# Kernel tuning notes

Hardware: AMD Instinct MI355X
Metric: run time of the kernel (lower is better)

Reference implementation:

```python
import jax, jax.numpy as jnp
import numpy as np


def _generate_anchors(anc, grid):
    # anc: (A,2) = (w,h); grid: (B,H,W,2) = (x,y) centers
    # -> anchors (B,A,H,W,4) = (x_tl, y_tl, x_br, y_br)
    centers = jnp.concatenate([grid, grid], axis=-1)[:, None, :, :, :]  # (B,1,H,W,4)
    half = 0.5 * jnp.stack([-anc[:, 0], -anc[:, 1], anc[:, 0], anc[:, 1]], axis=-1)  # (A,4)
    return centers + half[None, :, None, None, :]


def _generate_proposals_yolo(anchors, offsets):
    # anchors, offsets: (B,A,H,W,4) -> proposals (B,A,H,W,4)
    x_ca = 0.5 * (anchors[..., 0] + anchors[..., 2])
    y_ca = 0.5 * (anchors[..., 1] + anchors[..., 3])
    wa = anchors[..., 2] - anchors[..., 0]
    ha = anchors[..., 3] - anchors[..., 1]
    # YOLO transform: center shift is additive, size is log-space scale
    x_cp = x_ca + offsets[..., 0]
    y_cp = y_ca + offsets[..., 1]
    wp = wa * jnp.exp(offsets[..., 2])
    hp = ha * jnp.exp(offsets[..., 3])
    return jnp.stack([x_cp - 0.5 * wp, y_cp - 0.5 * hp,
                      x_cp + 0.5 * wp, y_cp + 0.5 * hp], axis=-1)


def _iou(proposals, bboxes):
    # proposals: (B,A,H,W,4); bboxes: (B,N,5) -> iou_mat (B, A*H*W, N)
    B = proposals.shape[0]
    p = proposals.reshape(B, -1, 1, 4)          # (B, AHW, 1, 4)
    b = bboxes[:, None, :, :4]                   # (B, 1,  N, 4)
    tl = jnp.maximum(p[..., :2], b[..., :2])     # (B, AHW, N, 2)
    br = jnp.minimum(p[..., 2:], b[..., 2:])
    no_inter = (tl[..., 0] > br[..., 0]) | (tl[..., 1] > br[..., 1])
    aoi = (br[..., 0] - tl[..., 0]) * (br[..., 1] - tl[..., 1])
    aoi = jnp.where(no_inter, 0.0, aoi)
    aop = (p[..., 2] - p[..., 0]) * (p[..., 3] - p[..., 1])  # (B, AHW, 1)
    aob = (b[..., 2] - b[..., 0]) * (b[..., 3] - b[..., 1])  # (B, 1,  N)
    return aoi / (aop + aob - aoi)


def setup_inputs() -> dict:
    key = jax.random.key(0)
    k1, k2, k3, k4 = jax.random.split(key, 4)
    B, A, H, W, N = 16, 9, 56, 56, 64
    anc = jax.random.uniform(k1, (A, 2), dtype=jnp.float32)          # anchor (w,h) shapes
    grid = jax.random.uniform(k2, (B, H, W, 2), dtype=jnp.float32)   # cell centers
    offsets = jax.random.normal(k3, (B, A, H, W, 4), dtype=jnp.float32)
    bboxes = jax.random.uniform(k4, (B, N, 5), dtype=jnp.float32)    # GT boxes (x1,y1,x2,y2,cls)
    return {"anc": anc, "grid": grid, "offsets": offsets, "bboxes": bboxes}


def reference(anc, grid, offsets, bboxes):
    anchors = _generate_anchors(anc, grid)
    proposals = _generate_proposals_yolo(anchors, offsets)
    iou_mat = _iou(proposals, bboxes)
    return iou_mat
```

## Files before the change

### kernel.cpp

```cpp
#include <hip/hip_runtime.h>
#include <hip/hip_bf16.h>


constexpr int B_ = 16;
constexpr int A_ = 9;
constexpr int H_ = 56;
constexpr int W_ = 56;
constexpr int N_ = 64;
constexpr int HW_ = H_ * W_;
constexpr int P_ = A_ * HW_;
constexpr int BLOCK = 192;
constexpr int BLKS_PER_BATCH = P_ / BLOCK;

__global__ __launch_bounds__(BLOCK) void ssd_iou_kernel(
    const float* __restrict__ anc,
    const float* __restrict__ grid,
    const float* __restrict__ offsets,
    const float* __restrict__ bboxes,
    float* __restrict__ out)
{
    __shared__ float4 s_box[BLOCK];
    __shared__ float  s_aop[BLOCK];

    const int t  = threadIdx.x;
    const int b  = blockIdx.x / BLKS_PER_BATCH;
    const int lb = blockIdx.x - b * BLKS_PER_BATCH;
    const int p0 = lb * BLOCK;

    {
        const int lp = p0 + t;
        const int a  = lp / HW_;
        const int hw = lp - a * HW_;
        const int gp = b * P_ + lp;

        const float4 off = reinterpret_cast<const float4*>(offsets)[gp];
        const float2 g   = reinterpret_cast<const float2*>(grid)[b * HW_ + hw];
        const float  aw  = anc[2 * a + 0];
        const float  ah  = anc[2 * a + 1];

        const float xc = g.x + off.x;
        const float yc = g.y + off.y;
        const float wp = aw * __expf(off.z);
        const float hp = ah * __expf(off.w);

        float4 box;
        box.x = xc - 0.5f * wp;
        box.y = yc - 0.5f * hp;
        box.z = xc + 0.5f * wp;
        box.w = yc + 0.5f * hp;
        s_box[t] = box;
        s_aop[t] = wp * hp;
    }
    __syncthreads();

    const int wave = t >> 6;
    const int lane = t & 63;

    const float* bb = bboxes + ((size_t)(b * N_ + lane)) * 5;
    const float bx0 = bb[0];
    const float by0 = bb[1];
    const float bx1 = bb[2];
    const float by1 = bb[3];
    const float aob = (bx1 - bx0) * (by1 - by0);

    const int   pbase = wave * 64;
    float* orow = out + ((size_t)(b * P_ + p0 + pbase)) * N_ + lane;

    #pragma unroll 8
    for (int j = 0; j < 64; ++j) {
        const float4 pr  = s_box[pbase + j];
        const float  aop = s_aop[pbase + j];

        const float tlx = fmaxf(pr.x, bx0);
        const float tly = fmaxf(pr.y, by0);
        const float brx = fminf(pr.z, bx1);
        const float bry = fminf(pr.w, by1);

        const float iw  = fmaxf(brx - tlx, 0.0f);
        const float ih  = fmaxf(bry - tly, 0.0f);
        const float aoi = iw * ih;

        const float denom = aop + aob - aoi;
        const float iou   = aoi * __frcp_rn(denom);

        __builtin_nontemporal_store(iou, orow + (size_t)j * N_);
    }
}

extern "C" void kernel_launch(void* const* d_in, const int* in_sizes, int n_in,
                              void* d_out, int out_size, void* d_ws, size_t ws_size,
                              hipStream_t stream) {
    const float* anc     = (const float*)d_in[0];
    const float* grid    = (const float*)d_in[1];
    const float* offsets = (const float*)d_in[2];
    const float* bboxes  = (const float*)d_in[3];
    float* out = (float*)d_out;

    const int nblocks = B_ * BLKS_PER_BATCH;
    ssd_iou_kernel<<<nblocks, BLOCK, 0, stream>>>(anc, grid, offsets, bboxes, out);
}
```

Before: 136.9 us.

## Vectorize IoU output stores to 128-bit by giving each lane four boxes

Each lane now computes four consecutive GT boxes for one proposal and writes them with a single 128-bit nontemporal store, in place of one 32-bit store per lane per proposal. The per-proposal area is recomputed from the shared box, so the separate shared-memory area array is gone. The correctly rounded reciprocal is replaced with the raw hardware rcp builtin. This aims to cut store instruction count on a write-bound kernel, at the cost of more registers per lane and slightly different rounding in the division.

```diff
diff --git a/kernel.cpp b/kernel.cpp
--- a/kernel.cpp
+++ b/kernel.cpp
@@ -12,6 +12,8 @@
 constexpr int BLOCK = 192;
 constexpr int BLKS_PER_BATCH = P_ / BLOCK;
 
+typedef float floatx4 __attribute__((ext_vector_type(4)));
+
 __global__ __launch_bounds__(BLOCK) void ssd_iou_kernel(
     const float* __restrict__ anc,
     const float* __restrict__ grid,
@@ -20,7 +22,6 @@
     float* __restrict__ out)
 {
     __shared__ float4 s_box[BLOCK];
-    __shared__ float  s_aop[BLOCK];
 
     const int t  = threadIdx.x;
     const int b  = blockIdx.x / BLKS_PER_BATCH;
@@ -49,41 +50,51 @@
         box.z = xc + 0.5f * wp;
         box.w = yc + 0.5f * hp;
         s_box[t] = box;
-        s_aop[t] = wp * hp;
     }
     __syncthreads();
 
     const int wave = t >> 6;
     const int lane = t & 63;
+    const int q    = lane >> 4;
+    const int g    = lane & 15;
 
-    const float* bb = bboxes + ((size_t)(b * N_ + lane)) * 5;
-    const float bx0 = bb[0];
-    const float by0 = bb[1];
-    const float bx1 = bb[2];
-    const float by1 = bb[3];
-    const float aob = (bx1 - bx0) * (by1 - by0);
+    float bx0[4], by0[4], bx1[4], by1[4], aob[4];
+    #pragma unroll
+    for (int k = 0; k < 4; ++k) {
+        const float* bb = bboxes + ((size_t)(b * N_ + 4 * g + k)) * 5;
+        bx0[k] = bb[0];
+        by0[k] = bb[1];
+        bx1[k] = bb[2];
+        by1[k] = bb[3];
+        aob[k] = (bx1[k] - bx0[k]) * (by1[k] - by0[k]);
+    }
 
-    const int   pbase = wave * 64;
-    float* orow = out + ((size_t)(b * P_ + p0 + pbase)) * N_ + lane;
+    const int pbase = wave * 64;
+    float* obase = out + ((size_t)(b * P_ + p0 + pbase + q)) * N_ + 4 * g;
 
     #pragma unroll 8
-    for (int j = 0; j < 64; ++j) {
-        const float4 pr  = s_box[pbase + j];
-        const float  aop = s_aop[pbase + j];
+    for (int j = 0; j < 16; ++j) {
+        const float4 pr = s_box[pbase + 4 * j + q];
+        const float aop = (pr.z - pr.x) * (pr.w - pr.y);
 
-        const float tlx = fmaxf(pr.x, bx0);
-        const float tly = fmaxf(pr.y, by0);
-        const float brx = fminf(pr.z, bx1);
-        const float bry = fminf(pr.w, by1);
+        floatx4 res;
+        #pragma unroll
+        for (int k = 0; k < 4; ++k) {
+            const float tlx = fmaxf(pr.x, bx0[k]);
+            const float tly = fmaxf(pr.y, by0[k]);
+            const float brx = fminf(pr.z, bx1[k]);
+            const float bry = fminf(pr.w, by1[k]);
 
-        const float iw  = fmaxf(brx - tlx, 0.0f);
-        const float ih  = fmaxf(bry - tly, 0.0f);
-        const float aoi = iw * ih;
+            const float iw  = fmaxf(brx - tlx, 0.0f);
+            const float ih  = fmaxf(bry - tly, 0.0f);
+            const float aoi = iw * ih;
 
-        const float denom = aop + aob - aoi;
-        const float iou   = aoi * __frcp_rn(denom);
+            const float denom = aop + aob[k] - aoi;
+            res[k] = aoi * __builtin_amdgcn_rcpf(denom);
+        }
 
-        __builtin_nontemporal_store(iou, orow + (size_t)j * N_);
+        __builtin_nontemporal_store(res,
+            reinterpret_cast<floatx4*>(obase + (size_t)(4 * j) * N_));
     }
 }
 
```

Result: no change. 138.0 us (+0.8%).
